# Performance work log

Hardware: AMD Instinct MI355X
Metric: run time of the kernel (lower is better)

## Reference

```python
import jax, jax.numpy as jnp
import numpy as np

B, S, D = 2, 2048, 1024
H = 16
DK = D // H


def setup_inputs() -> dict:
    key = jax.random.key(0)
    ks = jax.random.split(key, 5)
    std = np.sqrt(2.0 / (D + D))
    x = jax.random.normal(ks[0], (B, S, D), dtype=jnp.float32)
    wq = jax.random.normal(ks[1], (D, D), dtype=jnp.float32) * std
    wk = jax.random.normal(ks[2], (D, D), dtype=jnp.float32) * std
    wv = jax.random.normal(ks[3], (D, D), dtype=jnp.float32) * std
    wo = jax.random.normal(ks[4], (D, D), dtype=jnp.float32) * std
    return {"x": x, "wq": wq, "wk": wk, "wv": wv, "wo": wo}


def reference(x, wq, wk, wv, wo):
    # Linear: y = x @ W.T  (weight stored as [d_out, d_in])
    q = jnp.einsum("bsd,ed->bse", x, wq)
    k = jnp.einsum("bsd,ed->bse", x, wk)
    v = jnp.einsum("bsd,ed->bse", x, wv)
    # split heads: [B, S, H*DK] -> [B, H, S, DK]
    q = q.reshape(B, S, H, DK).transpose(0, 2, 1, 3)
    k = k.reshape(B, S, H, DK).transpose(0, 2, 1, 3)
    v = v.reshape(B, S, H, DK).transpose(0, 2, 1, 3)
    scale = 1.0 / jnp.sqrt(jnp.asarray(DK, dtype=x.dtype))
    scores = jnp.einsum("bhqd,bhkd->bhqk", q, k) * scale  # [B,H,S,S]
    causal = jnp.tril(jnp.ones((S, S), dtype=bool))
    scores = jnp.where(causal, scores, -jnp.inf)
    attn = jax.nn.softmax(scores, axis=-1)
    out = jnp.einsum("bhqk,bhkd->bhqd", attn, v)  # [B,H,S,DK]
    out = out.transpose(0, 2, 1, 3).reshape(B, S, D)
    return jnp.einsum("bsd,ed->bse", out, wo)
```

## Files before the change

### kernel.cpp

```cpp
#include <hip/hip_runtime.h>
#include <hip/hip_bf16.h>
#include <cstdint>

#define B_ 2
#define S_ 2048
#define D_ 1024
#define H_ 16
#define DK_ 64

#define LOG2E_S 0.18033688f

typedef __attribute__((ext_vector_type(8))) short bf16x8;
typedef __attribute__((ext_vector_type(4))) float f32x4;

__device__ __forceinline__ unsigned short f2bf(float f) {
  unsigned u = __float_as_uint(f);
  u = (u + 0x7FFFu + ((u >> 16) & 1u)) >> 16;
  return (unsigned short)u;
}

__device__ __forceinline__ unsigned short f2bf_hw(float f) {
  __hip_bfloat16 h = __float2bfloat16(f);
  return *reinterpret_cast<unsigned short*>(&h);
}

typedef __attribute__((address_space(1))) void gv_t;
typedef __attribute__((address_space(3))) void lv_t;
__device__ __forceinline__ void gl16(const void* g, void* l) {
  __builtin_amdgcn_global_load_lds((gv_t*)g, (lv_t*)l, 16, 0, 0);
}

__device__ __forceinline__ void stage8w(const unsigned short* gbase, size_t ldg,
                                        unsigned short* lds, int wave, int lane) {
  const int lr = lane >> 3;
  const int col8 = (lane & 7) ^ lr;
  gl16(gbase + (size_t)(wave * 8 + lr) * ldg + col8 * 8, lds + wave * 512);
}

__device__ __forceinline__ bf16x8 rdswz(const unsigned short* lds, int row, int col) {
  return *(const bf16x8*)&lds[row * 64 + (col ^ ((row & 7) << 3))];
}

__global__ void cvt_all_kernel(const float* __restrict__ x,
                               const float* __restrict__ w0, const float* __restrict__ w1,
                               const float* __restrict__ w2, const float* __restrict__ w3,
                               unsigned short* __restrict__ xo,
                               unsigned short* __restrict__ o0, unsigned short* __restrict__ o1,
                               unsigned short* __restrict__ o2, unsigned short* __restrict__ o3) {
  const int NX4 = 1 << 20;
  const int TOT = 1 << 21;
  for (int i = blockIdx.x * blockDim.x + threadIdx.x; i < TOT; i += gridDim.x * blockDim.x) {
    const float* in;
    unsigned short* out;
    int off;
    if (i < NX4) {
      in = x; out = xo; off = i;
    } else {
      int j = i - NX4;
      int mat = j >> 18;
      off = j & ((1 << 18) - 1);
      in = (mat == 0) ? w0 : (mat == 1) ? w1 : (mat == 2) ? w2 : w3;
      out = (mat == 0) ? o0 : (mat == 1) ? o1 : (mat == 2) ? o2 : o3;
    }
    const float4 v = reinterpret_cast<const float4*>(in)[off];
    ushort4 o;
    o.x = f2bf(v.x); o.y = f2bf(v.y); o.z = f2bf(v.z); o.w = f2bf(v.w);
    reinterpret_cast<ushort4*>(out)[off] = o;
  }
}

#define BM 128
#define BK 64

template <typename OutT, bool TV2, int BNv, bool SCALEQ>
__global__ __launch_bounds__(256) void gemm_bt(
    const unsigned short* __restrict__ A,
    const unsigned short* __restrict__ B0, const unsigned short* __restrict__ B1,
    const unsigned short* __restrict__ B2,
    OutT* __restrict__ C0, OutT* __restrict__ C1, OutT* __restrict__ C2,
    int M, int N, int K) {
  constexpr int NFRAG = BNv / 32;
  __shared__ unsigned short lA[BM * BK];
  __shared__ unsigned short lB[BNv * BK];
  const int tid = threadIdx.x;
  const int wave = tid >> 6, lane = tid & 63;
  const int l16 = lane & 15, lqq = lane >> 4;
  const int wr = wave >> 1, wc = wave & 1;
  const int lr = lane >> 3;
  const int col8 = ((lane & 7) ^ lr) * 8;

  const int tilesPerMat = N / BNv;
  const int bx = blockIdx.x;
  const int mat = bx / tilesPerMat;
  const int n0 = (bx % tilesPerMat) * BNv;
  const unsigned short* Bm = (mat == 0) ? B0 : (mat == 1) ? B1 : B2;
  OutT* C = (mat == 0) ? C0 : (mat == 1) ? C1 : C2;
  const int m0 = blockIdx.y * BM;

  f32x4 acc[4][NFRAG] = {};

  for (int k0 = 0; k0 < K; k0 += BK) {
    __syncthreads();
#pragma unroll
    for (int c = wave; c < 16; c += 4)
      gl16(A + (size_t)(m0 + c * 8 + lr) * K + k0 + col8, &lA[c * 512]);
#pragma unroll
    for (int c = wave; c < BNv / 8; c += 4)
      gl16(Bm + (size_t)(n0 + c * 8 + lr) * K + k0 + col8, &lB[c * 512]);
    __syncthreads();
#pragma unroll
    for (int kk = 0; kk < BK / 32; ++kk) {
      bf16x8 af[4], bfr[NFRAG];
#pragma unroll
      for (int m = 0; m < 4; ++m)
        af[m] = rdswz(lA, wr * 64 + m * 16 + l16, kk * 32 + lqq * 8);
#pragma unroll
      for (int n = 0; n < NFRAG; ++n)
        bfr[n] = rdswz(lB, wc * (BNv / 2) + n * 16 + l16, kk * 32 + lqq * 8);
      __builtin_amdgcn_s_setprio(1);
#pragma unroll
      for (int m = 0; m < 4; ++m)
#pragma unroll
        for (int n = 0; n < NFRAG; ++n)
          acc[m][n] = __builtin_amdgcn_mfma_f32_16x16x32_bf16(af[m], bfr[n], acc[m][n], 0, 0, 0);
      __builtin_amdgcn_s_setprio(0);
    }
  }

  if (TV2 && mat == 2) {
    unsigned short* Vt = (unsigned short*)C;
#pragma unroll
    for (int m = 0; m < 4; ++m)
#pragma unroll
      for (int n = 0; n < NFRAG; ++n) {
        int r0 = m0 + wr * 64 + m * 16 + lqq * 4;
        int cidx = n0 + wc * (BNv / 2) + n * 16 + l16;
        int bb = r0 >> 11, s = r0 & 2047;
        int h = cidx >> 6, dv = cidx & 63;
        ushort4 o;
        o.x = f2bf(acc[m][n][0]); o.y = f2bf(acc[m][n][1]);
        o.z = f2bf(acc[m][n][2]); o.w = f2bf(acc[m][n][3]);
        *(ushort4*)(Vt + ((size_t)((bb * H_ + h) * DK_ + dv)) * S_ + s) = o;
      }
  } else {
    const float cscale = (SCALEQ && mat == 0) ? LOG2E_S : 1.0f;
#pragma unroll
    for (int m = 0; m < 4; ++m)
#pragma unroll
      for (int n = 0; n < NFRAG; ++n)
#pragma unroll
        for (int j = 0; j < 4; ++j) {
          int r = m0 + wr * 64 + m * 16 + lqq * 4 + j;
          int cidx = n0 + wc * (BNv / 2) + n * 16 + l16;
          float v = acc[m][n][j] * cscale;
          if constexpr (sizeof(OutT) == 4) C[(size_t)r * N + cidx] = v;
          else C[(size_t)r * N + cidx] = f2bf(v);
        }
  }
}

__global__ __launch_bounds__(512) void attn_kernel(
    const unsigned short* __restrict__ Qg, const unsigned short* __restrict__ Kg,
    const unsigned short* __restrict__ Vtg, unsigned short* __restrict__ Og) {
  __shared__ unsigned short sQ[2][64 * 64];
  __shared__ unsigned short sK[2][64 * 64];
  __shared__ unsigned short sVt[2][64 * 64];
  __shared__ unsigned short sP[8][2][16 * 64];
  const int tid = threadIdx.x, wave = tid >> 6, lane = tid & 63;
  const int side = wave >> 2, wq = wave & 3;
  const int l16 = lane & 15, lq = lane >> 4;
  const int id = blockIdx.x;
  const int bh = (id & 7) * 4 + ((id >> 3) & 3);
  const int g = (id >> 5) & 7;
  const int i = (id < 256) ? (15 - g) : g;
  const int b = bh >> 4, h = bh & 15;
  const int qtA = 2 * i, qtB = 2 * i + 1;
  const int qt_s = side ? qtB : qtA;
  const int NT = i + 1;
  const size_t tokbase = (size_t)b * S_ * D_ + h * DK_;
  const unsigned short* VtB = Vtg + (size_t)(b * H_ + h) * DK_ * S_;
  unsigned short (*sPw)[16 * 64] = sP[wave];

  stage8w(Qg + tokbase + (size_t)(qtA * 64) * D_, D_, sQ[0], wave, lane);
  stage8w(Qg + tokbase + (size_t)(qtB * 64) * D_, D_, sQ[1], wave, lane);
  stage8w(Kg + tokbase, D_, sK[0], wave, lane);
  stage8w(Kg + tokbase + (size_t)64 * D_, D_, sK[1], wave, lane);
  stage8w(VtB, S_, sVt[0], wave, lane);
  stage8w(VtB + 64, S_, sVt[1], wave, lane);
  __syncthreads();
  bf16x8 aq0 = rdswz(sQ[side], wq * 16 + l16, lq * 8);
  bf16x8 aq1 = rdswz(sQ[side], wq * 16 + l16, 32 + lq * 8);

  const float THR2 = 11.5416f;
  const short ONE_BF = 0x3F80;
  const bf16x8 vones = {ONE_BF, ONE_BF, ONE_BF, ONE_BF, ONE_BF, ONE_BF, ONE_BF, ONE_BF};
  float m_run[4] = {-1e30f, -1e30f, -1e30f, -1e30f};
  f32x4 sum_acc = {};
  f32x4 o_acc[4] = {};

#pragma unroll 1
  for (int kt = 0; kt < NT; ++kt) {
    const bool last = (kt == NT - 1);
    float p[8][4];

#pragma unroll
    for (int sub = 0; sub < 2; ++sub) {
      const bool skip = (sub == 1) && (side == 0) && last;
      if (!skip) {
        __builtin_amdgcn_s_setprio(1);
#pragma unroll
        for (int nb = 0; nb < 4; ++nb) {
          bf16x8 bk0 = rdswz(sK[sub], nb * 16 + l16, lq * 8);
          bf16x8 bk1 = rdswz(sK[sub], nb * 16 + l16, 32 + lq * 8);
          f32x4 a = {};
          a = __builtin_amdgcn_mfma_f32_16x16x32_bf16(aq0, bk0, a, 0, 0, 0);
          a = __builtin_amdgcn_mfma_f32_16x16x32_bf16(aq1, bk1, a, 0, 0, 0);
#pragma unroll
          for (int j = 0; j < 4; ++j) p[sub * 4 + nb][j] = a[j];
        }
        __builtin_amdgcn_s_setprio(0);
      } else {
#pragma unroll
        for (int nb = 0; nb < 4; ++nb)
#pragma unroll
          for (int j = 0; j < 4; ++j) p[sub * 4 + nb][j] = -1e30f;
      }
    }

    __syncthreads();
    if (kt + 1 < NT) {
      stage8w(Kg + tokbase + (size_t)((kt + 1) * 128) * D_, D_, sK[0], wave, lane);
      stage8w(Kg + tokbase + (size_t)((kt + 1) * 128 + 64) * D_, D_, sK[1], wave, lane);
    }

    if (last) {
      if (side == 0) {
#pragma unroll
        for (int nb = 0; nb < 4; ++nb)
#pragma unroll
          for (int j = 0; j < 4; ++j) {
            int kidx = nb * 16 + l16;
            int qidx = wq * 16 + lq * 4 + j;
            if (kidx > qidx) p[nb][j] = -1e30f;
          }
      } else {
#pragma unroll
        for (int nb = 0; nb < 4; ++nb)
#pragma unroll
          for (int j = 0; j < 4; ++j) {
            int kidx = nb * 16 + l16;
            int qidx = wq * 16 + lq * 4 + j;
            if (kidx > qidx) p[4 + nb][j] = -1e30f;
          }
      }
    }

    float pmax[4];
    bool ok = true;
#pragma unroll
    for (int j = 0; j < 4; ++j) {
      float r = p[0][j];
#pragma unroll
      for (int nbb = 1; nbb < 8; ++nbb) r = fmaxf(r, p[nbb][j]);
      pmax[j] = r;
      ok = ok && (r <= m_run[j] + THR2);
    }
    if (!__all((int)ok)) {
#pragma unroll
      for (int j = 0; j < 4; ++j) {
        float r = pmax[j];
#pragma unroll
        for (int d = 1; d < 16; d <<= 1) r = fmaxf(r, __shfl_xor(r, d));
        float mn = fmaxf(m_run[j], r);
        float alpha = exp2f(m_run[j] - mn);
        m_run[j] = mn;
        sum_acc[j] *= alpha;
#pragma unroll
        for (int nb = 0; nb < 4; ++nb) o_acc[nb][j] *= alpha;
      }
    }
#pragma unroll
    for (int j = 0; j < 4; ++j) {
      const int rw = lq * 4 + j;
#pragma unroll
      for (int nbb = 0; nbb < 8; ++nbb) {
        float e = exp2f(p[nbb][j] - m_run[j]);
        sPw[nbb >> 2][rw * 64 + (((nbb & 3) * 16 + l16) ^ ((rw & 7) << 3))] = f2bf_hw(e);
      }
    }

    __builtin_amdgcn_s_setprio(1);
#pragma unroll
    for (int sub = 0; sub < 2; ++sub)
#pragma unroll
      for (int kk = 0; kk < 2; ++kk) {
        bf16x8 ap = rdswz(sPw[sub], l16, kk * 32 + lq * 8);
        sum_acc = __builtin_amdgcn_mfma_f32_16x16x32_bf16(ap, vones, sum_acc, 0, 0, 0);
#pragma unroll
        for (int nb = 0; nb < 4; ++nb) {
          bf16x8 bv = rdswz(sVt[sub], nb * 16 + l16, kk * 32 + lq * 8);
          o_acc[nb] = __builtin_amdgcn_mfma_f32_16x16x32_bf16(ap, bv, o_acc[nb], 0, 0, 0);
        }
      }
    __builtin_amdgcn_s_setprio(0);

    __syncthreads();
    if (kt + 1 < NT) {
      stage8w(VtB + (kt + 1) * 128, S_, sVt[0], wave, lane);
      stage8w(VtB + (kt + 1) * 128 + 64, S_, sVt[1], wave, lane);
    }
  }

#pragma unroll
  for (int j = 0; j < 4; ++j) {
    float inv = 1.f / sum_acc[j];
#pragma unroll
    for (int nb = 0; nb < 4; ++nb) {
      int r = qt_s * 64 + wq * 16 + lq * 4 + j;
      Og[tokbase + (size_t)r * D_ + nb * 16 + l16] = f2bf(o_acc[nb][j] * inv);
    }
  }
}

extern "C" void kernel_launch(void* const* d_in, const int* in_sizes, int n_in,
                              void* d_out, int out_size, void* d_ws, size_t ws_size,
                              hipStream_t stream) {
  const float* x = (const float*)d_in[0];
  const float* wq = (const float*)d_in[1];
  const float* wk = (const float*)d_in[2];
  const float* wv = (const float*)d_in[3];
  const float* wo = (const float*)d_in[4];
  float* out = (float*)d_out;

  char* ws = (char*)d_ws;
  const size_t MB = 1024 * 1024;
  unsigned short* xb  = (unsigned short*)(ws + 0);
  unsigned short* wqb = (unsigned short*)(ws + 8 * MB);
  unsigned short* wkb = (unsigned short*)(ws + 10 * MB);
  unsigned short* wvb = (unsigned short*)(ws + 12 * MB);
  unsigned short* wob = (unsigned short*)(ws + 14 * MB);
  unsigned short* Qb  = (unsigned short*)(ws + 16 * MB);
  unsigned short* Kb  = (unsigned short*)(ws + 24 * MB);
  unsigned short* Vtb = (unsigned short*)(ws + 32 * MB);
  unsigned short* AOb = (unsigned short*)(ws + 40 * MB);

  const int M = B_ * S_;
  const int N = D_, K = D_;

  cvt_all_kernel<<<dim3(2048), 256, 0, stream>>>(
      x, wq, wk, wv, wo, xb, wqb, wkb, wvb, wob);

  gemm_bt<unsigned short, true, 128, true><<<dim3(3 * (N / 128), M / BM), 256, 0, stream>>>(
      xb, wqb, wkb, wvb, Qb, Kb, Vtb, M, N, K);

  attn_kernel<<<dim3(512), 512, 0, stream>>>(Qb, Kb, Vtb, AOb);

  gemm_bt<float, false, 64, false><<<dim3(N / 64, M / BM), 256, 0, stream>>>(
      AOb, wob, wob, wob, out, out, out, M, N, K);
}
```

Before: 105.5 us.

## Widen attention KV tile to 256 keys and load Q directly into registers

```diff
diff --git a/kernel.cpp b/kernel.cpp
--- a/kernel.cpp
+++ b/kernel.cpp
@@ -162,10 +162,9 @@
 __global__ __launch_bounds__(512) void attn_kernel(
     const unsigned short* __restrict__ Qg, const unsigned short* __restrict__ Kg,
     const unsigned short* __restrict__ Vtg, unsigned short* __restrict__ Og) {
-  __shared__ unsigned short sQ[2][64 * 64];
-  __shared__ unsigned short sK[2][64 * 64];
-  __shared__ unsigned short sVt[2][64 * 64];
-  __shared__ unsigned short sP[8][2][16 * 64];
+  __shared__ unsigned short sK[4][64 * 64];
+  __shared__ unsigned short sVt[4][64 * 64];
+  __shared__ unsigned short sP[8][16 * 64];
   const int tid = threadIdx.x, wave = tid >> 6, lane = tid & 63;
   const int side = wave >> 2, wq = wave & 3;
   const int l16 = lane & 15, lq = lane >> 4;
@@ -176,20 +175,21 @@
   const int b = bh >> 4, h = bh & 15;
   const int qtA = 2 * i, qtB = 2 * i + 1;
   const int qt_s = side ? qtB : qtA;
-  const int NT = i + 1;
+  const int NT = (2 * i + 5) >> 2;
   const size_t tokbase = (size_t)b * S_ * D_ + h * DK_;
   const unsigned short* VtB = Vtg + (size_t)(b * H_ + h) * DK_ * S_;
-  unsigned short (*sPw)[16 * 64] = sP[wave];
-
-  stage8w(Qg + tokbase + (size_t)(qtA * 64) * D_, D_, sQ[0], wave, lane);
-  stage8w(Qg + tokbase + (size_t)(qtB * 64) * D_, D_, sQ[1], wave, lane);
-  stage8w(Kg + tokbase, D_, sK[0], wave, lane);
-  stage8w(Kg + tokbase + (size_t)64 * D_, D_, sK[1], wave, lane);
-  stage8w(VtB, S_, sVt[0], wave, lane);
-  stage8w(VtB + 64, S_, sVt[1], wave, lane);
+  unsigned short* sPw = sP[wave];
+
+  const unsigned short* qrow = Qg + tokbase + (size_t)(qt_s * 64 + wq * 16 + l16) * D_;
+  bf16x8 aq0 = *(const bf16x8*)(qrow + lq * 8);
+  bf16x8 aq1 = *(const bf16x8*)(qrow + 32 + lq * 8);
+
+#pragma unroll
+  for (int s = 0; s < 4; ++s) {
+    stage8w(Kg + tokbase + (size_t)(s * 64) * D_, D_, sK[s], wave, lane);
+    stage8w(VtB + s * 64, S_, sVt[s], wave, lane);
+  }
   __syncthreads();
-  bf16x8 aq0 = rdswz(sQ[side], wq * 16 + l16, lq * 8);
-  bf16x8 aq1 = rdswz(sQ[side], wq * 16 + l16, 32 + lq * 8);
 
   const float THR2 = 11.5416f;
   const short ONE_BF = 0x3F80;
@@ -200,13 +200,11 @@
 
 #pragma unroll 1
   for (int kt = 0; kt < NT; ++kt) {
-    const bool last = (kt == NT - 1);
-    float p[8][4];
-
-#pragma unroll
-    for (int sub = 0; sub < 2; ++sub) {
-      const bool skip = (sub == 1) && (side == 0) && last;
-      if (!skip) {
+    float p[16][4];
+
+#pragma unroll
+    for (int sub = 0; sub < 4; ++sub) {
+      if (kt * 4 + sub <= qt_s) {
         __builtin_amdgcn_s_setprio(1);
 #pragma unroll
         for (int nb = 0; nb < 4; ++nb) {
@@ -229,28 +227,21 @@
 
     __syncthreads();
     if (kt + 1 < NT) {
-      stage8w(Kg + tokbase + (size_t)((kt + 1) * 128) * D_, D_, sK[0], wave, lane);
-      stage8w(Kg + tokbase + (size_t)((kt + 1) * 128 + 64) * D_, D_, sK[1], wave, lane);
-    }
-
-    if (last) {
-      if (side == 0) {
+#pragma unroll
+      for (int s = 0; s < 4; ++s)
+        stage8w(Kg + tokbase + (size_t)(((kt + 1) * 4 + s) * 64) * D_, D_, sK[s], wave, lane);
+    }
+
+#pragma unroll
+    for (int sub = 0; sub < 4; ++sub) {
+      if (kt * 4 + sub == qt_s) {
 #pragma unroll
         for (int nb = 0; nb < 4; ++nb)
 #pragma unroll
           for (int j = 0; j < 4; ++j) {
             int kidx = nb * 16 + l16;
             int qidx = wq * 16 + lq * 4 + j;
-            if (kidx > qidx) p[nb][j] = -1e30f;
-          }
-      } else {
-#pragma unroll
-        for (int nb = 0; nb < 4; ++nb)
-#pragma unroll
-          for (int j = 0; j < 4; ++j) {
-            int kidx = nb * 16 + l16;
-            int qidx = wq * 16 + lq * 4 + j;
-            if (kidx > qidx) p[4 + nb][j] = -1e30f;
+            if (kidx > qidx) p[sub * 4 + nb][j] = -1e30f;
           }
       }
     }
@@ -261,7 +252,7 @@
     for (int j = 0; j < 4; ++j) {
       float r = p[0][j];
 #pragma unroll
-      for (int nbb = 1; nbb < 8; ++nbb) r = fmaxf(r, p[nbb][j]);
+      for (int nbb = 1; nbb < 16; ++nbb) r = fmaxf(r, p[nbb][j]);
       pmax[j] = r;
       ok = ok && (r <= m_run[j] + THR2);
     }
@@ -280,34 +271,41 @@
       }
     }
 #pragma unroll
-    for (int j = 0; j < 4; ++j) {
-      const int rw = lq * 4 + j;
-#pragma unroll
-      for (int nbb = 0; nbb < 8; ++nbb) {
-        float e = exp2f(p[nbb][j] - m_run[j]);
-        sPw[nbb >> 2][rw * 64 + (((nbb & 3) * 16 + l16) ^ ((rw & 7) << 3))] = f2bf_hw(e);
-      }
-    }
-
-    __builtin_amdgcn_s_setprio(1);
-#pragma unroll
-    for (int sub = 0; sub < 2; ++sub)
-#pragma unroll
-      for (int kk = 0; kk < 2; ++kk) {
-        bf16x8 ap = rdswz(sPw[sub], l16, kk * 32 + lq * 8);
-        sum_acc = __builtin_amdgcn_mfma_f32_16x16x32_bf16(ap, vones, sum_acc, 0, 0, 0);
-#pragma unroll
-        for (int nb = 0; nb < 4; ++nb) {
-          bf16x8 bv = rdswz(sVt[sub], nb * 16 + l16, kk * 32 + lq * 8);
-          o_acc[nb] = __builtin_amdgcn_mfma_f32_16x16x32_bf16(ap, bv, o_acc[nb], 0, 0, 0);
+    for (int j = 0; j < 4; ++j)
+#pragma unroll
+      for (int nbb = 0; nbb < 16; ++nbb)
+        p[nbb][j] = exp2f(p[nbb][j] - m_run[j]);
+
+#pragma unroll
+    for (int sub = 0; sub < 4; ++sub) {
+      if (kt * 4 + sub <= qt_s) {
+#pragma unroll
+        for (int j = 0; j < 4; ++j) {
+          const int rw = lq * 4 + j;
+#pragma unroll
+          for (int nb = 0; nb < 4; ++nb)
+            sPw[rw * 64 + (((nb * 16 + l16) ^ ((rw & 7) << 3)))] = f2bf_hw(p[sub * 4 + nb][j]);
         }
-      }
-    __builtin_amdgcn_s_setprio(0);
+        __builtin_amdgcn_s_setprio(1);
+#pragma unroll
+        for (int kk = 0; kk < 2; ++kk) {
+          bf16x8 ap = rdswz(sPw, l16, kk * 32 + lq * 8);
+          sum_acc = __builtin_amdgcn_mfma_f32_16x16x32_bf16(ap, vones, sum_acc, 0, 0, 0);
+#pragma unroll
+          for (int nb = 0; nb < 4; ++nb) {
+            bf16x8 bv = rdswz(sVt[sub], nb * 16 + l16, kk * 32 + lq * 8);
+            o_acc[nb] = __builtin_amdgcn_mfma_f32_16x16x32_bf16(ap, bv, o_acc[nb], 0, 0, 0);
+          }
+        }
+        __builtin_amdgcn_s_setprio(0);
+      }
+    }
 
     __syncthreads();
     if (kt + 1 < NT) {
-      stage8w(VtB + (kt + 1) * 128, S_, sVt[0], wave, lane);
-      stage8w(VtB + (kt + 1) * 128 + 64, S_, sVt[1], wave, lane);
+#pragma unroll
+      for (int s = 0; s < 4; ++s)
+        stage8w(VtB + ((kt + 1) * 4 + s) * 64, S_, sVt[s], wave, lane);
     }
   }
 
```

Result: slower. 120.5 us (+14.3%).
